# Kernel tuning notes

Hardware: AMD Instinct MI355X
Metric: run time of the kernel (lower is better)

The kernel has to match this reference:

```python
import jax, jax.numpy as jnp
import numpy as np
from jax import lax

L, H, C, V, BLK = 6, 12, 768, 50257, 1024
B, T = 4, 1024
HD = C // H
EPS = 1e-5


def _norm(key, shape, scale=0.02):
    return jax.random.normal(key, shape, dtype=jnp.float32) * scale


def setup_inputs() -> dict:
    key = jax.random.key(0)
    ks = jax.random.split(key, 16)
    idx = jax.random.randint(ks[0], (B, T), 0, V)
    inp = {
        "idx": idx,
        "wte": _norm(ks[1], (V, C)),
        "wpe": _norm(ks[2], (BLK, C)),
        "ln1_s": jnp.ones((L, C)),
        "ln1_b": jnp.zeros((L, C)),
        "qkv_w": _norm(ks[3], (L, C, 3 * C)),
        "qkv_b": jnp.zeros((L, 3 * C)),
        "proj_w": _norm(ks[4], (L, C, C)),
        "proj_b": jnp.zeros((L, C)),
        "ln2_s": jnp.ones((L, C)),
        "ln2_b": jnp.zeros((L, C)),
        "fc_w": _norm(ks[5], (L, C, 4 * C)),
        "fc_b": jnp.zeros((L, 4 * C)),
        "fcp_w": _norm(ks[6], (L, 4 * C, C)),
        "fcp_b": jnp.zeros((L, C)),
        "lnf_s": jnp.ones((C,)),
        "lnf_b": jnp.zeros((C,)),
    }
    return inp


def layer_norm(x, s, b):
    mu = jnp.mean(x, axis=-1, keepdims=True)
    var = jnp.mean(jnp.square(x - mu), axis=-1, keepdims=True)
    return (x - mu) * lax.rsqrt(var + EPS) * s + b


def block(x, p):
    ln1_s, ln1_b, qkv_w, qkv_b, proj_w, proj_b, ln2_s, ln2_b, fc_w, fc_b, fcp_w, fcp_b = p
    Bx, Tx, Cx = x.shape
    h = layer_norm(x, ln1_s, ln1_b)
    qkv = h @ qkv_w + qkv_b  # [B,T,3C]
    q, k, v = jnp.split(qkv, 3, axis=-1)
    q = q.reshape(Bx, Tx, H, HD).swapaxes(1, 2)  # [B,H,T,hd]
    k = k.reshape(Bx, Tx, H, HD).swapaxes(1, 2)
    v = v.reshape(Bx, Tx, H, HD).swapaxes(1, 2)
    attn = jnp.einsum("bhqd,bhkd->bhqk", q, k) / jnp.sqrt(jnp.float32(HD))
    mask = jnp.tril(jnp.ones((Tx, Tx), dtype=bool))
    attn = jnp.where(mask, attn, -jnp.inf)
    attn = jax.nn.softmax(attn, axis=-1)
    y = jnp.einsum("bhqk,bhkd->bhqd", attn, v)
    y = y.swapaxes(1, 2).reshape(Bx, Tx, Cx)
    x = x + (y @ proj_w + proj_b)
    h = layer_norm(x, ln2_s, ln2_b)
    h = jax.nn.gelu(h @ fc_w + fc_b, approximate=True)
    x = x + (h @ fcp_w + fcp_b)
    return x


def reference(idx, wte, wpe, ln1_s, ln1_b, qkv_w, qkv_b, proj_w, proj_b,
              ln2_s, ln2_b, fc_w, fc_b, fcp_w, fcp_b, lnf_s, lnf_b):
    Tx = idx.shape[1]
    x = wte[idx] + wpe[:Tx][None]  # [B,T,C]
    params = (ln1_s, ln1_b, qkv_w, qkv_b, proj_w, proj_b,
              ln2_s, ln2_b, fc_w, fc_b, fcp_w, fcp_b)
    def step(carry, p):
        return block(carry, p), None
    x, _ = lax.scan(step, x, params)
    x = layer_norm(x, lnf_s, lnf_b)
    logits = x @ wte.T  # tied embedding attend
    return logits
```

## Files before the change

### kernel.cpp

```cpp
#include <hip/hip_runtime.h>
#include <math.h>

#define LNUM 6
#define HNUM 12
#define CDIM 768
#define VDIM 50257
#define BDIM 4
#define TDIM 1024
#define NTOK 4096

typedef __bf16 bf16;
typedef __bf16 bf16x8 __attribute__((ext_vector_type(8)));
typedef float  floatx4 __attribute__((ext_vector_type(4)));
typedef unsigned int u32;

__device__ inline void gload16(const bf16* gsrc, bf16* lds) {
  __builtin_amdgcn_global_load_lds(
      (const __attribute__((address_space(1))) u32*)gsrc,
      (__attribute__((address_space(3))) u32*)lds, 16, 0, 0);
}

__global__ void k_cvt_bf16(const float* __restrict__ in, bf16* __restrict__ out, long n) {
  long i = ((long)blockIdx.x * blockDim.x + threadIdx.x) * 4;
  long stride = (long)gridDim.x * blockDim.x * 4;
  for (; i < n; i += stride) {
    float4 v = *reinterpret_cast<const float4*>(in + i);
    bf16 b0 = (bf16)v.x, b1 = (bf16)v.y, b2 = (bf16)v.z, b3 = (bf16)v.w;
    ushort4 pk;
    pk.x = __builtin_bit_cast(unsigned short, b0);
    pk.y = __builtin_bit_cast(unsigned short, b1);
    pk.z = __builtin_bit_cast(unsigned short, b2);
    pk.w = __builtin_bit_cast(unsigned short, b3);
    *reinterpret_cast<ushort4*>(out + i) = pk;
  }
}

__global__ void k_transpose_cvt(const float* __restrict__ in, bf16* __restrict__ out, int K, int N) {
  __shared__ float tile[32][33];
  int n0 = blockIdx.x * 32, k0 = blockIdx.y * 32;
  int nx = threadIdx.x & 31, ty = threadIdx.x >> 5;
  #pragma unroll
  for (int p = 0; p < 4; ++p) {
    int k = ty + p * 8;
    tile[k][nx] = in[(size_t)(k0 + k) * N + n0 + nx];
  }
  __syncthreads();
  #pragma unroll
  for (int p = 0; p < 4; ++p) {
    int n = ty + p * 8;
    out[(size_t)(n0 + n) * K + k0 + nx] = (bf16)tile[nx][n];
  }
}

__global__ void k_embed(const int* __restrict__ idx, const float* __restrict__ wte,
                        const float* __restrict__ wpe, float* __restrict__ x) {
  int tok = blockIdx.x;
  int t = tok & (TDIM - 1);
  int id = idx[tok];
  const float* a = wte + (size_t)id * CDIM;
  const float* p = wpe + (size_t)t * CDIM;
  float* o = x + (size_t)tok * CDIM;
  for (int c = threadIdx.x; c < CDIM; c += 256) o[c] = a[c] + p[c];
}

__global__ __launch_bounds__(256) void k_layernorm(const float* __restrict__ x,
    const float* __restrict__ sc, const float* __restrict__ bi, bf16* __restrict__ out) {
  __shared__ float red[8];
  int row = blockIdx.x;
  const float* xr = x + (size_t)row * CDIM;
  int t = threadIdx.x;
  float v0 = xr[t], v1 = xr[t + 256], v2 = xr[t + 512];
  float s = v0 + v1 + v2;
  #pragma unroll
  for (int o = 32; o > 0; o >>= 1) s += __shfl_down(s, o);
  if ((t & 63) == 0) red[t >> 6] = s;
  __syncthreads();
  float mean = (red[0] + red[1] + red[2] + red[3]) * (1.0f / CDIM);
  float d0 = v0 - mean, d1 = v1 - mean, d2 = v2 - mean;
  float q = d0 * d0 + d1 * d1 + d2 * d2;
  #pragma unroll
  for (int o = 32; o > 0; o >>= 1) q += __shfl_down(q, o);
  if ((t & 63) == 0) red[4 + (t >> 6)] = q;
  __syncthreads();
  float var = (red[4] + red[5] + red[6] + red[7]) * (1.0f / CDIM);
  float rs = rsqrtf(var + 1e-5f);
  bf16* orow = out + (size_t)row * CDIM;
  orow[t]       = (bf16)(d0 * rs * sc[t]       + bi[t]);
  orow[t + 256] = (bf16)(d1 * rs * sc[t + 256] + bi[t + 256]);
  orow[t + 512] = (bf16)(d2 * rs * sc[t + 512] + bi[t + 512]);
}

__device__ inline float gelu_f(float x) {
  float x3 = x * x * x;
  return 0.5f * x * (1.0f + tanhf(0.7978845608028654f * (x + 0.044715f * x3)));
}

template<int TBM, int MI, int NI, int EPI>
__global__ __launch_bounds__(256) void k_gemm(
    const bf16* __restrict__ A, const bf16* __restrict__ Bt,
    const float* __restrict__ bias, const float* __restrict__ resid,
    float* __restrict__ Cf, bf16* __restrict__ Cb,
    int M, int N, int K) {
  constexpr int BN = 128;
  constexpr int WGN = BN / (NI * 16);
  constexpr int AI = TBM / 32;
  constexpr int BI = BN / 32;
  __shared__ __align__(16) bf16 As[TBM * 64];
  __shared__ __align__(16) bf16 Bs[BN * 64];
  const int m0 = blockIdx.x * TBM, n0 = blockIdx.y * BN;
  const int tid = threadIdx.x;
  const int lane = tid & 63, wave = tid >> 6;
  const int wr = wave / WGN, wc = wave % WGN;
  const int l8 = lane >> 3, s8 = lane & 7;
  const int g = lane >> 4, r16 = lane & 15;

  floatx4 acc[MI][NI] = {};

  const bf16* a_src = A + (size_t)(m0 + l8) * K + s8 * 8;
  const bf16* b_src = Bt + (size_t)(n0 + l8) * K + s8 * 8;

  for (int k0 = 0; k0 < K; k0 += 64) {
    #pragma unroll
    for (int t = 0; t < AI; ++t) {
      int row0 = wave * (TBM / 4) + t * 8;
      gload16(a_src + (size_t)row0 * K + k0, &As[row0 * 64]);
    }
    #pragma unroll
    for (int t = 0; t < BI; ++t) {
      int row0 = wave * 32 + t * 8;
      gload16(b_src + (size_t)row0 * K + k0, &Bs[row0 * 64]);
    }
    __syncthreads();
    #pragma unroll
    for (int kk = 0; kk < 2; ++kk) {
      bf16x8 af[MI], bfr[NI];
      #pragma unroll
      for (int i = 0; i < MI; ++i)
        af[i] = *reinterpret_cast<const bf16x8*>(&As[(wr * MI * 16 + i * 16 + r16) * 64 + g * 8 + kk * 32]);
      #pragma unroll
      for (int j = 0; j < NI; ++j)
        bfr[j] = *reinterpret_cast<const bf16x8*>(&Bs[(wc * NI * 16 + j * 16 + r16) * 64 + g * 8 + kk * 32]);
      #pragma unroll
      for (int i = 0; i < MI; ++i) {
        #pragma unroll
        for (int j = 0; j < NI; ++j)
          acc[i][j] = __builtin_amdgcn_mfma_f32_16x16x32_bf16(af[i], bfr[j], acc[i][j], 0, 0, 0);
      }
    }
    __syncthreads();
  }

  int mb = m0 + wr * MI * 16 + g * 4;
  int nb = n0 + wc * NI * 16 + r16;
  #pragma unroll
  for (int j = 0; j < NI; ++j) {
    int n = nb + j * 16;
    if (n >= N) continue;
    float bv = (EPI >= 2) ? bias[n] : 0.0f;
    #pragma unroll
    for (int i = 0; i < MI; ++i) {
      #pragma unroll
      for (int q = 0; q < 4; ++q) {
        int m = mb + i * 16 + q;
        float v = acc[i][j][q] + bv;
        size_t o = (size_t)m * N + n;
        if (EPI == 2)      Cf[o] = v + resid[o];
        else if (EPI == 3) Cb[o] = (bf16)gelu_f(v);
        else if (EPI == 4) Cb[o] = (bf16)v;
        else               Cf[o] = v;
      }
    }
  }
}

__global__ __launch_bounds__(256) void k_vtrans(const bf16* __restrict__ qkv, bf16* __restrict__ vt) {
  __shared__ bf16 tile[64][72];
  int bh = blockIdx.x, t0 = blockIdx.y * 64;
  int b = bh / HNUM, h = bh % HNUM;
  int tid = threadIdx.x;
  int r8 = tid >> 3, s8 = tid & 7;
  #pragma unroll
  for (int p = 0; p < 2; ++p) {
    int row = p * 32 + r8;
    uint4 v = *reinterpret_cast<const uint4*>(
        qkv + (size_t)(b * TDIM + t0 + row) * (3 * CDIM) + 2 * CDIM + h * 64 + s8 * 8);
    *reinterpret_cast<uint4*>(&tile[row][s8 * 8]) = v;
  }
  __syncthreads();
  int d = tid >> 2, q4 = tid & 3;
  #pragma unroll
  for (int half = 0; half < 2; ++half) {
    int t = q4 * 16 + half * 8;
    bf16x8 o;
    #pragma unroll
    for (int u = 0; u < 8; ++u) o[u] = tile[t + u][d];
    *reinterpret_cast<bf16x8*>(vt + (size_t)bh * (64 * TDIM) + (size_t)d * TDIM + t0 + t) = o;
  }
}

__global__ __launch_bounds__(256) void k_attn(const bf16* __restrict__ qkv,
                                              const bf16* __restrict__ vt,
                                              bf16* __restrict__ y) {
  __shared__ __align__(16) bf16 Ks[64 * 64];
  __shared__ __align__(16) bf16 Vs[64 * 64];
  __shared__ __align__(16) bf16 Ps[64 * 64];
  const int bh = blockIdx.x, qt = blockIdx.y;
  const int b = bh / HNUM, h = bh % HNUM;
  const int tid = threadIdx.x, lane = tid & 63, wave = tid >> 6;
  const int g = lane >> 4, r16 = lane & 15;
  const int w16 = wave * 16;
  const int r8 = tid >> 3, s8 = tid & 7;

  bf16x8 qf[2];
  {
    const bf16* qsrc = qkv + (size_t)(b * TDIM + qt * 64 + w16 + r16) * (3 * CDIM) + h * 64 + g * 8;
    qf[0] = *reinterpret_cast<const bf16x8*>(qsrc);
    qf[1] = *reinterpret_cast<const bf16x8*>(qsrc + 32);
  }

  float m_r[4], l_r[4];
  floatx4 yacc[4] = {};
  #pragma unroll
  for (int q = 0; q < 4; ++q) { m_r[q] = -1e30f; l_r[q] = 0.f; }

  for (int kt = 0; kt <= qt; ++kt) {
    __syncthreads();
    #pragma unroll
    for (int p = 0; p < 2; ++p) {
      int row = p * 32 + r8;
      uint4 kv = *reinterpret_cast<const uint4*>(
          qkv + (size_t)(b * TDIM + kt * 64 + row) * (3 * CDIM) + CDIM + h * 64 + s8 * 8);
      *reinterpret_cast<uint4*>(&Ks[row * 64 + ((s8 ^ (row & 7)) * 8)]) = kv;
      uint4 vv = *reinterpret_cast<const uint4*>(
          vt + (size_t)bh * (64 * TDIM) + (size_t)row * TDIM + kt * 64 + s8 * 8);
      *reinterpret_cast<uint4*>(&Vs[row * 64 + ((s8 ^ (row & 7)) * 8)]) = vv;
    }
    __syncthreads();

    floatx4 sa[4] = {};
    #pragma unroll
    for (int c = 0; c < 2; ++c) {
      bf16x8 kf[4];
      #pragma unroll
      for (int j = 0; j < 4; ++j) {
        int krow = j * 16 + r16;
        kf[j] = *reinterpret_cast<const bf16x8*>(&Ks[krow * 64 + (((g + 4 * c) ^ (krow & 7)) * 8)]);
      }
      #pragma unroll
      for (int j = 0; j < 4; ++j)
        sa[j] = __builtin_amdgcn_mfma_f32_16x16x32_bf16(qf[c], kf[j], sa[j], 0, 0, 0);
    }

    const bool diag = (kt == qt);
    float p_v[4][4];
    #pragma unroll
    for (int q = 0; q < 4; ++q) {
      int qrow = w16 + g * 4 + q;
      float mx = -1e30f;
      #pragma unroll
      for (int j = 0; j < 4; ++j) {
        float s = sa[j][q] * 0.125f;
        if (diag && (r16 + j * 16) > qrow) s = -1e30f;
        p_v[j][q] = s;
        mx = fmaxf(mx, s);
      }
      #pragma unroll
      for (int o = 1; o < 16; o <<= 1) mx = fmaxf(mx, __shfl_xor(mx, o));
      float mnew = fmaxf(m_r[q], mx);
      float ps = 0.f;
      #pragma unroll
      for (int j = 0; j < 4; ++j) {
        float p = __expf(p_v[j][q] - mnew);
        p_v[j][q] = p;
        ps += p;
      }
      #pragma unroll
      for (int o = 1; o < 16; o <<= 1) ps += __shfl_xor(ps, o);
      float alpha = __expf(m_r[q] - mnew);
      m_r[q] = mnew;
      l_r[q] = l_r[q] * alpha + ps;
      #pragma unroll
      for (int j = 0; j < 4; ++j) yacc[j][q] *= alpha;
      #pragma unroll
      for (int j = 0; j < 4; ++j) {
        int col = r16 + j * 16;
        Ps[qrow * 64 + (col ^ ((qrow & 7) << 3))] = (bf16)p_v[j][q];
      }
    }

    #pragma unroll
    for (int ks = 0; ks < 2; ++ks) {
      int prow = w16 + r16;
      bf16x8 pa = *reinterpret_cast<const bf16x8*>(&Ps[prow * 64 + (((g + 4 * ks) ^ (prow & 7)) * 8)]);
      #pragma unroll
      for (int j = 0; j < 4; ++j) {
        int vrow = j * 16 + r16;
        bf16x8 vb = *reinterpret_cast<const bf16x8*>(&Vs[vrow * 64 + (((g + 4 * ks) ^ (vrow & 7)) * 8)]);
        yacc[j] = __builtin_amdgcn_mfma_f32_16x16x32_bf16(pa, vb, yacc[j], 0, 0, 0);
      }
    }
  }

  #pragma unroll
  for (int q = 0; q < 4; ++q) {
    float inv = 1.0f / l_r[q];
    int tok = b * TDIM + qt * 64 + w16 + g * 4 + q;
    #pragma unroll
    for (int j = 0; j < 4; ++j)
      y[(size_t)tok * CDIM + h * 64 + r16 + j * 16] = (bf16)(yacc[j][q] * inv);
  }
}

extern "C" void kernel_launch(void* const* d_in, const int* in_sizes, int n_in,
                              void* d_out, int out_size, void* d_ws, size_t ws_size,
                              hipStream_t stream) {
  (void)in_sizes; (void)n_in; (void)out_size;
  const int*   idx    = (const int*)  d_in[0];
  const float* wte    = (const float*)d_in[1];
  const float* wpe    = (const float*)d_in[2];
  const float* ln1_s  = (const float*)d_in[3];
  const float* ln1_b  = (const float*)d_in[4];
  const float* qkv_w  = (const float*)d_in[5];
  const float* qkv_b  = (const float*)d_in[6];
  const float* proj_w = (const float*)d_in[7];
  const float* proj_b = (const float*)d_in[8];
  const float* ln2_s  = (const float*)d_in[9];
  const float* ln2_b  = (const float*)d_in[10];
  const float* fc_w   = (const float*)d_in[11];
  const float* fc_b   = (const float*)d_in[12];
  const float* fcp_w  = (const float*)d_in[13];
  const float* fcp_b  = (const float*)d_in[14];
  const float* lnf_s  = (const float*)d_in[15];
  const float* lnf_b  = (const float*)d_in[16];
  float* logits = (float*)d_out;

  char* base = (char*)d_ws;
  size_t off = 0;
  auto alloc = [&](size_t bytes) -> void* {
    void* p = base + off;
    off += (bytes + 255) & ~(size_t)255;
    return p;
  };
  bf16*  wte_bf = (bf16*) alloc((size_t)VDIM * CDIM * 2);
  bf16*  wq_t   = (bf16*) alloc((size_t)3 * CDIM * CDIM * 2);
  bf16*  wp_t   = (bf16*) alloc((size_t)CDIM * CDIM * 2);
  bf16*  wf_t   = (bf16*) alloc((size_t)4 * CDIM * CDIM * 2);
  bf16*  wfp_t  = (bf16*) alloc((size_t)4 * CDIM * CDIM * 2);
  float* x      = (float*)alloc((size_t)NTOK * CDIM * 4);
  bf16*  hb     = (bf16*) alloc((size_t)NTOK * CDIM * 2);
  bf16*  qkv_bf = (bf16*) alloc((size_t)NTOK * 3 * CDIM * 2);
  bf16*  vt     = (bf16*) alloc((size_t)BDIM * HNUM * 64 * TDIM * 2);
  bf16*  yb     = (bf16*) alloc((size_t)NTOK * CDIM * 2);
  bf16*  gb     = (bf16*) alloc((size_t)NTOK * 4 * CDIM * 2);
  if (off > ws_size) return;

  k_cvt_bf16<<<4096, 256, 0, stream>>>(wte, wte_bf, (long)VDIM * CDIM);
  k_embed<<<NTOK, 256, 0, stream>>>(idx, wte, wpe, x);

  for (int l = 0; l < LNUM; ++l) {
    k_transpose_cvt<<<dim3(3*CDIM/32, CDIM/32), 256, 0, stream>>>(qkv_w + (size_t)l*CDIM*3*CDIM, wq_t, CDIM, 3*CDIM);
    k_transpose_cvt<<<dim3(CDIM/32,   CDIM/32), 256, 0, stream>>>(proj_w + (size_t)l*CDIM*CDIM,  wp_t, CDIM, CDIM);
    k_transpose_cvt<<<dim3(4*CDIM/32, CDIM/32), 256, 0, stream>>>(fc_w  + (size_t)l*CDIM*4*CDIM, wf_t, CDIM, 4*CDIM);
    k_transpose_cvt<<<dim3(CDIM/32, 4*CDIM/32), 256, 0, stream>>>(fcp_w + (size_t)l*4*CDIM*CDIM, wfp_t, 4*CDIM, CDIM);

    k_layernorm<<<NTOK, 256, 0, stream>>>(x, ln1_s + l*CDIM, ln1_b + l*CDIM, hb);
    k_gemm<128,4,4,4><<<dim3(NTOK/128, 18), 256, 0, stream>>>(hb, wq_t, qkv_b + (size_t)l*3*CDIM, nullptr, nullptr, qkv_bf, NTOK, 3*CDIM, CDIM);
    k_vtrans<<<dim3(BDIM*HNUM, TDIM/64), 256, 0, stream>>>(qkv_bf, vt);
    k_attn<<<dim3(BDIM*HNUM, TDIM/64), 256, 0, stream>>>(qkv_bf, vt, yb);
    k_gemm<64,4,2,2><<<dim3(NTOK/64, 6), 256, 0, stream>>>(yb, wp_t, proj_b + (size_t)l*CDIM, x, x, nullptr, NTOK, CDIM, CDIM);
    k_layernorm<<<NTOK, 256, 0, stream>>>(x, ln2_s + l*CDIM, ln2_b + l*CDIM, hb);
    k_gemm<128,4,4,3><<<dim3(NTOK/128, 24), 256, 0, stream>>>(hb, wf_t, fc_b + (size_t)l*4*CDIM, nullptr, nullptr, gb, NTOK, 4*CDIM, CDIM);
    k_gemm<64,4,2,2><<<dim3(NTOK/64, 6), 256, 0, stream>>>(gb, wfp_t, fcp_b + (size_t)l*CDIM, x, x, nullptr, NTOK, CDIM, 4*CDIM);
  }

  k_layernorm<<<NTOK, 256, 0, stream>>>(x, lnf_s, lnf_b, hb);
  int ntile = (VDIM + 127) / 128;
  k_gemm<128,4,4,0><<<dim3(NTOK/128, ntile), 256, 0, stream>>>(hb, wte_bf, nullptr, nullptr, logits, nullptr, NTOK, VDIM, CDIM);
}
```

Baseline: 2.143 ms.

## Add 256x256 eight-wave pipelined GEMM for QKV, FC and LM-head matmuls

Result: faster. 2.049 ms (-4.4%).

```diff
diff --git a/kernel.cpp b/kernel.cpp
--- a/kernel.cpp
+++ b/kernel.cpp
@@ -93,6 +93,141 @@
 __device__ inline float gelu_f(float x) {
   float x3 = x * x * x;
   return 0.5f * x * (1.0f + tanhf(0.7978845608028654f * (x + 0.044715f * x3)));
+}
+
+template<int EPI>
+__global__ __launch_bounds__(512, 1) void k_gemm8(
+    const bf16* __restrict__ A, const bf16* __restrict__ Bt,
+    const float* __restrict__ bias,
+    float* __restrict__ Cf, bf16* __restrict__ Cb,
+    int N, int K) {
+  __shared__ __align__(16) bf16 lds[2][4][8192];
+  const int nwg = gridDim.x;
+  const int id = blockIdx.x;
+  const int swz = (id & 7) * (nwg >> 3) + (id >> 3);
+  const int m0 = (swz & 15) * 256;
+  const int n0 = (swz >> 4) * 256;
+  const int tid = threadIdx.x, lane = tid & 63, wave = tid >> 6;
+  const int wr = wave >> 2, wc = wave & 3;
+  const int g = lane >> 4, r16 = lane & 15;
+  const int numK = K >> 6;
+
+  const int srow = wave * 16 + (lane >> 2);
+  const int scol = (lane & 3) * 8;
+  const bf16* aptr0 = A  + (size_t)(m0 + srow) * K + scol;
+  const bf16* aptr1 = A  + (size_t)(m0 + srow + 128) * K + scol;
+  const bf16* bptr0 = Bt + (size_t)(n0 + srow) * K + scol;
+  const bf16* bptr1 = Bt + (size_t)(n0 + srow + 128) * K + scol;
+  const int a_off = (wr * 128 + r16) * 32 + g * 8;
+  const int b_off = (wc * 64 + r16) * 32 + g * 8;
+
+  floatx4 acc[8][4] = {};
+
+#define STAGE_HALF(H) do {                                                \
+    int H_ = (H);                                                         \
+    if (H_ < numK * 4) {                                                  \
+      int tau_ = H_ >> 2, h_ = H_ & 3;                                    \
+      int isA_ = (h_ & 1), kk_ = (h_ >> 1) & 1;                           \
+      bf16* dst_ = &lds[tau_ & 1][h_][wave * 512];                        \
+      int ko_ = tau_ * 64 + kk_ * 32;                                     \
+      gload16((isA_ ? aptr0 : bptr0) + ko_, dst_);                        \
+      gload16((isA_ ? aptr1 : bptr1) + ko_, dst_ + 4096);                 \
+    } } while (0)
+
+  STAGE_HALF(0); STAGE_HALF(1); STAGE_HALF(2); STAGE_HALF(3);
+  STAGE_HALF(4); STAGE_HALF(5); STAGE_HALF(6);
+  asm volatile("s_waitcnt vmcnt(6)" ::: "memory");
+  __builtin_amdgcn_s_barrier();
+
+  for (int t = 0; t < numK; ++t) {
+    const int p = t & 1;
+    const int Hb = 4 * t + 7;
+    bf16x8 af[4], bfr[4];
+
+    #pragma unroll
+    for (int j = 0; j < 4; ++j) bfr[j] = *(const bf16x8*)&lds[p][0][b_off + j * 512];
+    #pragma unroll
+    for (int i = 0; i < 4; ++i) af[i] = *(const bf16x8*)&lds[p][1][a_off + i * 512];
+    STAGE_HALF(Hb);
+    __builtin_amdgcn_s_barrier();
+    asm volatile("s_waitcnt lgkmcnt(0)" ::: "memory");
+    __builtin_amdgcn_s_setprio(1);
+    #pragma unroll
+    for (int i = 0; i < 4; ++i)
+      #pragma unroll
+      for (int j = 0; j < 4; ++j)
+        acc[i][j] = __builtin_amdgcn_mfma_f32_16x16x32_bf16(af[i], bfr[j], acc[i][j], 0, 0, 0);
+    __builtin_amdgcn_s_setprio(0);
+    __builtin_amdgcn_s_barrier();
+
+    #pragma unroll
+    for (int i = 0; i < 4; ++i) af[i] = *(const bf16x8*)&lds[p][1][a_off + (i + 4) * 512];
+    STAGE_HALF(Hb + 1);
+    __builtin_amdgcn_s_barrier();
+    asm volatile("s_waitcnt lgkmcnt(0)" ::: "memory");
+    __builtin_amdgcn_s_setprio(1);
+    #pragma unroll
+    for (int i = 0; i < 4; ++i)
+      #pragma unroll
+      for (int j = 0; j < 4; ++j)
+        acc[i + 4][j] = __builtin_amdgcn_mfma_f32_16x16x32_bf16(af[i], bfr[j], acc[i + 4][j], 0, 0, 0);
+    __builtin_amdgcn_s_setprio(0);
+    __builtin_amdgcn_s_barrier();
+
+    #pragma unroll
+    for (int j = 0; j < 4; ++j) bfr[j] = *(const bf16x8*)&lds[p][2][b_off + j * 512];
+    #pragma unroll
+    for (int i = 0; i < 4; ++i) af[i] = *(const bf16x8*)&lds[p][3][a_off + i * 512];
+    STAGE_HALF(Hb + 2);
+    __builtin_amdgcn_s_barrier();
+    asm volatile("s_waitcnt lgkmcnt(0)" ::: "memory");
+    __builtin_amdgcn_s_setprio(1);
+    #pragma unroll
+    for (int i = 0; i < 4; ++i)
+      #pragma unroll
+      for (int j = 0; j < 4; ++j)
+        acc[i][j] = __builtin_amdgcn_mfma_f32_16x16x32_bf16(af[i], bfr[j], acc[i][j], 0, 0, 0);
+    __builtin_amdgcn_s_setprio(0);
+    __builtin_amdgcn_s_barrier();
+
+    #pragma unroll
+    for (int i = 0; i < 4; ++i) af[i] = *(const bf16x8*)&lds[p][3][a_off + (i + 4) * 512];
+    STAGE_HALF(Hb + 3);
+    __builtin_amdgcn_s_barrier();
+    asm volatile("s_waitcnt lgkmcnt(0)" ::: "memory");
+    __builtin_amdgcn_s_setprio(1);
+    #pragma unroll
+    for (int i = 0; i < 4; ++i)
+      #pragma unroll
+      for (int j = 0; j < 4; ++j)
+        acc[i + 4][j] = __builtin_amdgcn_mfma_f32_16x16x32_bf16(af[i], bfr[j], acc[i + 4][j], 0, 0, 0);
+    __builtin_amdgcn_s_setprio(0);
+    if (t + 2 < numK) { asm volatile("s_waitcnt vmcnt(6)" ::: "memory"); }
+    else              { asm volatile("s_waitcnt vmcnt(0)" ::: "memory"); }
+    __builtin_amdgcn_s_barrier();
+  }
+#undef STAGE_HALF
+
+  const int mb = m0 + wr * 128 + g * 4;
+  const int nb = n0 + wc * 64 + r16;
+  #pragma unroll
+  for (int nf = 0; nf < 4; ++nf) {
+    int n = nb + nf * 16;
+    if (EPI == 0 && n >= N) continue;
+    float bv = (EPI >= 3) ? bias[n] : 0.0f;
+    #pragma unroll
+    for (int mf = 0; mf < 8; ++mf) {
+      #pragma unroll
+      for (int q = 0; q < 4; ++q) {
+        int m = mb + mf * 16 + q;
+        float v = acc[mf][nf][q] + bv;
+        size_t o = (size_t)m * N + n;
+        if (EPI == 3)      Cb[o] = (bf16)gelu_f(v);
+        else if (EPI == 4) Cb[o] = (bf16)v;
+        else               Cf[o] = v;
+      }
+    }
+  }
 }
 
 template<int TBM, int MI, int NI, int EPI>
@@ -364,16 +499,16 @@
     k_transpose_cvt<<<dim3(CDIM/32, 4*CDIM/32), 256, 0, stream>>>(fcp_w + (size_t)l*4*CDIM*CDIM, wfp_t, 4*CDIM, CDIM);
 
     k_layernorm<<<NTOK, 256, 0, stream>>>(x, ln1_s + l*CDIM, ln1_b + l*CDIM, hb);
-    k_gemm<128,4,4,4><<<dim3(NTOK/128, 18), 256, 0, stream>>>(hb, wq_t, qkv_b + (size_t)l*3*CDIM, nullptr, nullptr, qkv_bf, NTOK, 3*CDIM, CDIM);
+    k_gemm8<4><<<16 * 9, 512, 0, stream>>>(hb, wq_t, qkv_b + (size_t)l*3*CDIM, nullptr, qkv_bf, 3*CDIM, CDIM);
     k_vtrans<<<dim3(BDIM*HNUM, TDIM/64), 256, 0, stream>>>(qkv_bf, vt);
     k_attn<<<dim3(BDIM*HNUM, TDIM/64), 256, 0, stream>>>(qkv_bf, vt, yb);
     k_gemm<64,4,2,2><<<dim3(NTOK/64, 6), 256, 0, stream>>>(yb, wp_t, proj_b + (size_t)l*CDIM, x, x, nullptr, NTOK, CDIM, CDIM);
     k_layernorm<<<NTOK, 256, 0, stream>>>(x, ln2_s + l*CDIM, ln2_b + l*CDIM, hb);
-    k_gemm<128,4,4,3><<<dim3(NTOK/128, 24), 256, 0, stream>>>(hb, wf_t, fc_b + (size_t)l*4*CDIM, nullptr, nullptr, gb, NTOK, 4*CDIM, CDIM);
+    k_gemm8<3><<<16 * 12, 512, 0, stream>>>(hb, wf_t, fc_b + (size_t)l*4*CDIM, nullptr, gb, 4*CDIM, CDIM);
     k_gemm<64,4,2,2><<<dim3(NTOK/64, 6), 256, 0, stream>>>(gb, wfp_t, fcp_b + (size_t)l*CDIM, x, x, nullptr, NTOK, CDIM, 4*CDIM);
   }
 
   k_layernorm<<<NTOK, 256, 0, stream>>>(x, lnf_s, lnf_b, hb);
-  int ntile = (VDIM + 127) / 128;
-  k_gemm<128,4,4,0><<<dim3(NTOK/128, ntile), 256, 0, stream>>>(hb, wte_bf, nullptr, nullptr, logits, nullptr, NTOK, VDIM, CDIM);
-}
+  int ntile = (VDIM + 255) / 256;
+  k_gemm8<0><<<16 * ntile, 512, 0, stream>>>(hb, wte_bf, nullptr, logits, nullptr, VDIM, CDIM);
+}
```
